# Kernel optimization log

Hardware: AMD Instinct MI355X
Metric: run time of the kernel (lower is better)

Reference implementation:

```python
import jax, jax.numpy as jnp
import numpy as np

NUM_HEADS = 10
LN_EPS = 1e-5

def setup_inputs() -> dict:
    key = jax.random.key(0)
    ks = jax.random.split(key, 8)
    B, H, N, D, Dt = 256, 200, 64, 640, 256
    s = 0.02
    return {
        'clicked_news': jax.random.normal(ks[0], (B, H, D), jnp.float32),
        'clicked_topics': jax.random.normal(ks[1], (B, H, Dt), jnp.float32),
        'cand_topics': jax.random.normal(ks[2], (B, N, Dt), jnp.float32),
        'Wq': jax.random.normal(ks[3], (D, Dt), jnp.float32) * s,
        'bq': jnp.zeros((D,), jnp.float32),
        'Wk': jax.random.normal(ks[4], (D, Dt), jnp.float32) * s,
        'bk': jnp.zeros((D,), jnp.float32),
        'Wv': jax.random.normal(ks[5], (D, D), jnp.float32) * s,
        'bv': jnp.zeros((D,), jnp.float32),
        'Wg': jax.random.normal(ks[6], (D, D), jnp.float32) * s,
        'bg': jnp.zeros((D,), jnp.float32),
        'ln_gamma': jnp.ones((D,), jnp.float32),
        'ln_beta': jnp.zeros((D,), jnp.float32),
    }

def reference(clicked_news, clicked_topics, cand_topics, Wq, bq, Wk, bk, Wv, bv, Wg, bg, ln_gamma, ln_beta):
    B, H, D = clicked_news.shape
    N = cand_topics.shape[1]
    nh = NUM_HEADS
    hd = D // nh
    scale = jnp.sqrt(jnp.asarray(D, clicked_news.dtype))

    Qf = cand_topics @ Wq.T + bq            # [B, N, D]
    Kf = clicked_topics @ Wk.T + bk         # [B, H, D]
    # V projection feeds `weighted`, which is dead code w.r.t. outputs; omitted.

    Q = Qf.reshape(B, N, nh, hd)
    K = Kf.reshape(B, H, nh, hd)
    scores = jnp.einsum('bnhd,bmhd->bhnm', Q, K) / scale   # [B, nh, N, H]
    attn = jax.nn.softmax(scores, axis=-1)                 # dropout is identity in eval

    # query weighting: softmax over candidates of ||Q||
    query_weights = jax.nn.softmax(jnp.linalg.norm(Qf, axis=-1), axis=1)   # [B, N]
    agg = (attn.sum(axis=1) * query_weights[:, :, None]).sum(axis=1)       # [B, H]
    attn_weights_agg = jax.nn.softmax(agg, axis=-1)                        # [B, H]

    weighted_clicked = attn_weights_agg[:, :, None] * clicked_news         # [B, H, D]
    gate = jax.nn.sigmoid(weighted_clicked @ Wg.T + bg)
    out = gate * weighted_clicked + (1.0 - gate) * clicked_news

    mu = out.mean(axis=-1, keepdims=True)
    var = out.var(axis=-1, keepdims=True)
    out = (out - mu) / jnp.sqrt(var + LN_EPS) * ln_gamma + ln_beta
    return out, attn_weights_agg
```

## Files before the change

kernel.cpp:

```cpp
#include <hip/hip_runtime.h>
#include <math.h>

#define B_  256
#define H_  200
#define N_  64
#define D_  640
#define DT_ 256
#define NH_ 10
#define HD_ 64
#define MT_ 13
#define MH_ 25600

typedef __attribute__((ext_vector_type(8))) short bf16x8;
typedef __attribute__((ext_vector_type(4))) float f32x4;

__device__ __forceinline__ float wave_reduce_sum(float v) {
    #pragma unroll
    for (int m = 32; m > 0; m >>= 1) v += __shfl_xor(v, m);
    return v;
}
__device__ __forceinline__ float wave_reduce_max(float v) {
    #pragma unroll
    for (int m = 32; m > 0; m >>= 1) v = fmaxf(v, __shfl_xor(v, m));
    return v;
}
__device__ __forceinline__ float red16_sum(float v) {
    #pragma unroll
    for (int m = 1; m < 16; m <<= 1) v += __shfl_xor(v, m);
    return v;
}
__device__ __forceinline__ float red16_max(float v) {
    #pragma unroll
    for (int m = 1; m < 16; m <<= 1) v = fmaxf(v, __shfl_xor(v, m));
    return v;
}
__device__ __forceinline__ short f2bf(float x) {
    unsigned u = __float_as_uint(x);
    unsigned r = (u + 0x7fffu + ((u >> 16) & 1u)) >> 16;
    return (short)r;
}
__device__ __forceinline__ float bf2f(short s) {
    return __uint_as_float(((unsigned)(unsigned short)s) << 16);
}

__device__ __forceinline__ void gload_lds16(const void* g, void* lds) {
    __builtin_amdgcn_global_load_lds(
        (const __attribute__((address_space(1))) void*)g,
        (__attribute__((address_space(3))) void*)lds, 16, 0, 0);
}

__global__ __launch_bounds__(256) void convert_w(
    const float* __restrict__ src, short* __restrict__ dst, int n)
{
    for (int i = blockIdx.x * 256 + threadIdx.x; i < n; i += gridDim.x * 256)
        dst[i] = f2bf(src[i]);
}

__global__ __launch_bounds__(256, 3) void gemm_bt(
    const float* __restrict__ A, int lda,
    const short* __restrict__ Wb, int ldb,
    const float* __restrict__ bias,
    short* __restrict__ Y, int nkc)
{
    __shared__ float A_f[128 * 64];
    __shared__ short B_lds[128 * 64];
    const int t = threadIdx.x;
    const int lane = t & 63, w = t >> 6;
    const int wm = w >> 1, wn = w & 1;
    const int r16 = lane & 15, g = lane >> 4;
    const int lb = (blockIdx.x & 7) * ((int)gridDim.x >> 3) + (blockIdx.x >> 3);
    const int row0 = (lb / 5) * 128;
    const int col0 = (lb % 5) * 128;

    f32x4 acc[4][4];
    #pragma unroll
    for (int ct = 0; ct < 4; ++ct)
        #pragma unroll
        for (int rt = 0; rt < 4; ++rt) acc[ct][rt] = (f32x4){0.f,0.f,0.f,0.f};

    for (int k = 0; k < nkc; ++k) {
        const int k0 = k * 64;
        #pragma unroll
        for (int j = 0; j < 8; ++j) {
            const int u = t + j * 256;
            const int row = u >> 4, jj = u & 15;
            gload_lds16(A + (long)(row0 + row) * lda + k0 + ((jj ^ (row & 7)) << 2),
                        (char*)A_f + u * 16);
        }
        #pragma unroll
        for (int j = 0; j < 4; ++j) {
            const int u = t + j * 256;
            const int col = u >> 3, jj = u & 7;
            gload_lds16(Wb + (long)(col0 + col) * ldb + k0 + ((jj ^ (col & 7)) << 3),
                        (char*)B_lds + u * 16);
        }
        __syncthreads();

        #pragma unroll
        for (int kk = 0; kk < 2; ++kk) {
            bf16x8 a[4];
            #pragma unroll
            for (int rt = 0; rt < 4; ++rt) {
                const int row = wm * 64 + rt * 16 + r16;
                const int s = kk * 8 + g * 2;
                float4 f0 = *(const float4*)(A_f + row * 64 + ((s ^ (row & 7)) << 2));
                float4 f1 = *(const float4*)(A_f + row * 64 + (((s + 1) ^ (row & 7)) << 2));
                bf16x8 av;
                av[0] = f2bf(f0.x); av[1] = f2bf(f0.y); av[2] = f2bf(f0.z); av[3] = f2bf(f0.w);
                av[4] = f2bf(f1.x); av[5] = f2bf(f1.y); av[6] = f2bf(f1.z); av[7] = f2bf(f1.w);
                a[rt] = av;
            }
            bf16x8 b[4];
            #pragma unroll
            for (int ct = 0; ct < 4; ++ct) {
                const int col = wn * 64 + ct * 16 + r16;
                const int sb = kk * 4 + g;
                b[ct] = *(const bf16x8*)(B_lds + col * 64 + ((sb ^ (col & 7)) << 3));
            }
            #pragma unroll
            for (int ct = 0; ct < 4; ++ct)
                #pragma unroll
                for (int rt = 0; rt < 4; ++rt)
                    acc[ct][rt] = __builtin_amdgcn_mfma_f32_16x16x32_bf16(
                                      a[rt], b[ct], acc[ct][rt], 0, 0, 0);
        }
        __syncthreads();
    }

    #pragma unroll
    for (int ct = 0; ct < 4; ++ct) {
        const int col = col0 + wn * 64 + ct * 16 + r16;
        const float bv = bias ? bias[col] : 0.f;
        #pragma unroll
        for (int rt = 0; rt < 4; ++rt)
            #pragma unroll
            for (int i = 0; i < 4; ++i)
                Y[(long)(row0 + wm * 64 + rt * 16 + g * 4 + i) * D_ + col] =
                    f2bf(acc[ct][rt][i] + bv);
    }
}

__global__ __launch_bounds__(512, 2) void attn2(
    const short* __restrict__ Qb, const short* __restrict__ Kb,
    float* __restrict__ aw, float* __restrict__ out_tail)
{
    __shared__ float qn_l[N_];
    __shared__ float qw_l[N_];
    __shared__ float aggp[8][MT_ * 16];
    __shared__ float red2[2];
    const int t = threadIdx.x;
    const int lane = t & 63, w = t >> 6;
    const int wm = w & 3, hh = w >> 2;
    const int r16 = lane & 15, g = lane >> 4;
    const int b = blockIdx.x;

    if (hh == 0) {
        const short* qrow = Qb + ((long)(b * N_ + wm * 16 + r16)) * D_ + g * 160;
        float ss = 0.f;
        #pragma unroll
        for (int j = 0; j < 20; ++j) {
            bf16x8 v = *(const bf16x8*)(qrow + j * 8);
            #pragma unroll
            for (int e = 0; e < 8; ++e) { float f = bf2f(v[e]); ss += f * f; }
        }
        ss += __shfl_xor(ss, 16);
        ss += __shfl_xor(ss, 32);
        if (g == 0) qn_l[wm * 16 + r16] = ss;
    }
    __syncthreads();
    if (w == 0) {
        float v = sqrtf(qn_l[lane]);
        float mx = wave_reduce_max(v);
        float e = __expf(v - mx);
        float s = wave_reduce_sum(e);
        qw_l[lane] = e / s;
    }
    __syncthreads();

    float qwr[4];
    #pragma unroll
    for (int i = 0; i < 4; ++i) qwr[i] = qw_l[wm * 16 + g * 4 + i];

    const float inv_scale = 0.0395284707521047f;
    float aggl[MT_];
    #pragma unroll
    for (int mt = 0; mt < MT_; ++mt) aggl[mt] = 0.f;

    for (int hi = 0; hi < 5; ++hi) {
        const int h = hh * 5 + hi;
        const short* qbase = Qb + ((long)(b * N_ + wm * 16 + r16)) * D_ + h * HD_ + g * 8;
        bf16x8 a0 = *(const bf16x8*)(qbase);
        bf16x8 a1 = *(const bf16x8*)(qbase + 32);
        bf16x8 kb0[MT_], kb1[MT_];
        #pragma unroll
        for (int mt = 0; mt < MT_; ++mt) {
            const short* kbase = Kb + ((long)(b * H_ + mt * 16 + r16)) * D_ + h * HD_ + g * 8;
            kb0[mt] = *(const bf16x8*)(kbase);
            kb1[mt] = *(const bf16x8*)(kbase + 32);
        }
        f32x4 acc[MT_];
        #pragma unroll
        for (int mt = 0; mt < MT_; ++mt) {
            f32x4 z = {0.f,0.f,0.f,0.f};
            z = __builtin_amdgcn_mfma_f32_16x16x32_bf16(a0, kb0[mt], z, 0, 0, 0);
            z = __builtin_amdgcn_mfma_f32_16x16x32_bf16(a1, kb1[mt], z, 0, 0, 0);
            acc[mt] = z;
        }
        const bool tailok = (r16 < 8);
        float mx[4] = {-INFINITY, -INFINITY, -INFINITY, -INFINITY};
        #pragma unroll
        for (int mt = 0; mt < MT_; ++mt) {
            const bool valid = (mt < 12) || tailok;
            #pragma unroll
            for (int i = 0; i < 4; ++i)
                if (valid) mx[i] = fmaxf(mx[i], acc[mt][i]);
        }
        #pragma unroll
        for (int i = 0; i < 4; ++i) mx[i] = red16_max(mx[i]);
        float sum[4] = {0.f, 0.f, 0.f, 0.f};
        #pragma unroll
        for (int mt = 0; mt < MT_; ++mt) {
            const bool valid = (mt < 12) || tailok;
            #pragma unroll
            for (int i = 0; i < 4; ++i) {
                float e = valid ? __expf((acc[mt][i] - mx[i]) * inv_scale) : 0.f;
                acc[mt][i] = e;
                sum[i] += e;
            }
        }
        float fct[4];
        #pragma unroll
        for (int i = 0; i < 4; ++i) fct[i] = qwr[i] / red16_sum(sum[i]);
        #pragma unroll
        for (int mt = 0; mt < MT_; ++mt)
            aggl[mt] += acc[mt][0] * fct[0] + acc[mt][1] * fct[1]
                      + acc[mt][2] * fct[2] + acc[mt][3] * fct[3];
    }
    #pragma unroll
    for (int mt = 0; mt < MT_; ++mt) {
        aggl[mt] += __shfl_xor(aggl[mt], 16);
        aggl[mt] += __shfl_xor(aggl[mt], 32);
    }
    if (g == 0) {
        #pragma unroll
        for (int mt = 0; mt < MT_; ++mt) aggp[w][mt * 16 + r16] = aggl[mt];
    }
    __syncthreads();
    if (t < MT_ * 16) {
        float v = 0.f;
        #pragma unroll
        for (int j = 0; j < 8; ++j) v += aggp[j][t];
        aggp[0][t] = v;
    }
    __syncthreads();
    if (w == 0) {
        float v0 = aggp[0][lane], v1 = aggp[0][lane + 64], v2 = aggp[0][lane + 128];
        const bool has3 = lane < (H_ - 192);
        float v3 = has3 ? aggp[0][lane + 192] : -INFINITY;
        float mx = wave_reduce_max(fmaxf(fmaxf(v0, v1), fmaxf(v2, v3)));
        float s = __expf(v0 - mx) + __expf(v1 - mx) + __expf(v2 - mx)
                + (has3 ? __expf(v3 - mx) : 0.f);
        s = wave_reduce_sum(s);
        if (lane == 0) { red2[0] = mx; red2[1] = s; }
    }
    __syncthreads();
    if (t < H_) {
        float v = __expf(aggp[0][t] - red2[0]) / red2[1];
        aw[b * H_ + t] = v;
        out_tail[b * H_ + t] = v;
    }
}

__global__ __launch_bounds__(256) void blendln(
    const float* __restrict__ cl, const short* __restrict__ Z,
    const float* __restrict__ aw, const float* __restrict__ bg,
    const float* __restrict__ gamma, const float* __restrict__ beta,
    float* __restrict__ out)
{
    const int t = threadIdx.x;
    const int lane = t & 63, w = t >> 6;
    const int row = blockIdx.x * 4 + w;
    const float awr = aw[row];
    const long base = (long)row * D_;

    float o[10];
    float s = 0.f, sq = 0.f;
    #pragma unroll
    for (int i = 0; i < 10; ++i) {
        const int col = lane + 64 * i;
        const float y = bf2f(Z[base + col]);
        const float c = cl[base + col];
        const float z = awr * y + bg[col];
        const float gt = 1.f / (1.f + __expf(-z));
        const float ov = c * (1.f + gt * (awr - 1.f));
        o[i] = ov; s += ov; sq += ov * ov;
    }
    s  = wave_reduce_sum(s);
    sq = wave_reduce_sum(sq);
    const float mu  = s * (1.f / D_);
    const float var = sq * (1.f / D_) - mu * mu;
    const float ri  = 1.0f / sqrtf(var + 1e-5f);
    #pragma unroll
    for (int i = 0; i < 10; ++i) {
        const int col = lane + 64 * i;
        out[base + col] = (o[i] - mu) * ri * gamma[col] + beta[col];
    }
}

extern "C" void kernel_launch(void* const* d_in, const int* in_sizes, int n_in,
                              void* d_out, int out_size, void* d_ws, size_t ws_size,
                              hipStream_t stream) {
    const float* clicked_news   = (const float*)d_in[0];
    const float* clicked_topics = (const float*)d_in[1];
    const float* cand_topics    = (const float*)d_in[2];
    const float* Wq = (const float*)d_in[3];
    const float* bq = (const float*)d_in[4];
    const float* Wk = (const float*)d_in[5];
    const float* bk = (const float*)d_in[6];
    const float* Wg = (const float*)d_in[9];
    const float* bg = (const float*)d_in[10];
    const float* ln_gamma = (const float*)d_in[11];
    const float* ln_beta  = (const float*)d_in[12];

    float* out = (float*)d_out;
    float* ws  = (float*)d_ws;

    float* aw   = ws;
    short* Wq_b = (short*)(aw + (long)B_ * H_);
    short* Wk_b = Wq_b + (long)D_ * DT_;
    short* Wg_b = Wk_b + (long)D_ * DT_;
    short* Qb   = Wg_b + (long)D_ * D_;
    short* Z    = Qb;
    short* Kb = (short*)d_out;
    float* out_tail = out + (long)B_ * H_ * D_;

    convert_w<<<128, 256, 0, stream>>>(Wq, Wq_b, D_ * DT_);
    convert_w<<<128, 256, 0, stream>>>(Wk, Wk_b, D_ * DT_);
    convert_w<<<256, 256, 0, stream>>>(Wg, Wg_b, D_ * D_);

    gemm_bt<<<640, 256, 0, stream>>>(cand_topics, DT_, Wq_b, DT_, bq, Qb, 4);
    gemm_bt<<<2000, 256, 0, stream>>>(clicked_topics, DT_, Wk_b, DT_, bk, Kb, 4);
    attn2<<<B_, 512, 0, stream>>>(Qb, Kb, aw, out_tail);

    for (int h = 0; h < 2; ++h) {
        const long off = (long)h * MH_;
        gemm_bt<<<1000, 256, 0, stream>>>(clicked_news + off * D_, D_,
                                          Wg_b, D_, nullptr, Z, 10);
        blendln<<<MH_ / 4, 256, 0, stream>>>(
            clicked_news + off * D_, Z, aw + off, bg, ln_gamma, ln_beta,
            out + off * D_);
    }
}
```

Measured before the change: 289.1 us.

## Double-buffer gemm_bt LDS tiles with half-size K chunks to overlap loads

The GEMM main loop now uses two LDS buffers with 32-wide K slices and prefetches the next slice while computing on the current one, with one barrier per iteration instead of two. The K chunk is halved so the total LDS footprint stays the same and occupancy is preserved, and call sites double the chunk count to match. The swizzle on the B tile changes for the narrower rows. The aim is to hide global-to-LDS load latency behind MFMA work, at the cost of twice as many loop iterations with fewer MFMAs each.

```diff
diff --git a/kernel.cpp b/kernel.cpp
--- a/kernel.cpp
+++ b/kernel.cpp
@@ -62,8 +62,8 @@
     const float* __restrict__ bias,
     short* __restrict__ Y, int nkc)
 {
-    __shared__ float A_f[128 * 64];
-    __shared__ short B_lds[128 * 64];
+    __shared__ float A_f[2][128 * 32];
+    __shared__ short B_l[2][128 * 32];
     const int t = threadIdx.x;
     const int lane = t & 63, w = t >> 6;
     const int wm = w >> 1, wn = w & 1;
@@ -78,52 +78,58 @@
         #pragma unroll
         for (int rt = 0; rt < 4; ++rt) acc[ct][rt] = (f32x4){0.f,0.f,0.f,0.f};
 
-    for (int k = 0; k < nkc; ++k) {
-        const int k0 = k * 64;
-        #pragma unroll
-        for (int j = 0; j < 8; ++j) {
-            const int u = t + j * 256;
-            const int row = u >> 4, jj = u & 15;
-            gload_lds16(A + (long)(row0 + row) * lda + k0 + ((jj ^ (row & 7)) << 2),
-                        (char*)A_f + u * 16);
-        }
+    auto STAGE = [&](int bi, int k) {
+        const int k0 = k * 32;
         #pragma unroll
         for (int j = 0; j < 4; ++j) {
             const int u = t + j * 256;
-            const int col = u >> 3, jj = u & 7;
-            gload_lds16(Wb + (long)(col0 + col) * ldb + k0 + ((jj ^ (col & 7)) << 3),
-                        (char*)B_lds + u * 16);
-        }
-        __syncthreads();
-
-        #pragma unroll
-        for (int kk = 0; kk < 2; ++kk) {
-            bf16x8 a[4];
-            #pragma unroll
-            for (int rt = 0; rt < 4; ++rt) {
-                const int row = wm * 64 + rt * 16 + r16;
-                const int s = kk * 8 + g * 2;
-                float4 f0 = *(const float4*)(A_f + row * 64 + ((s ^ (row & 7)) << 2));
-                float4 f1 = *(const float4*)(A_f + row * 64 + (((s + 1) ^ (row & 7)) << 2));
-                bf16x8 av;
-                av[0] = f2bf(f0.x); av[1] = f2bf(f0.y); av[2] = f2bf(f0.z); av[3] = f2bf(f0.w);
-                av[4] = f2bf(f1.x); av[5] = f2bf(f1.y); av[6] = f2bf(f1.z); av[7] = f2bf(f1.w);
-                a[rt] = av;
-            }
-            bf16x8 b[4];
-            #pragma unroll
-            for (int ct = 0; ct < 4; ++ct) {
-                const int col = wn * 64 + ct * 16 + r16;
-                const int sb = kk * 4 + g;
-                b[ct] = *(const bf16x8*)(B_lds + col * 64 + ((sb ^ (col & 7)) << 3));
-            }
-            #pragma unroll
-            for (int ct = 0; ct < 4; ++ct)
-                #pragma unroll
-                for (int rt = 0; rt < 4; ++rt)
-                    acc[ct][rt] = __builtin_amdgcn_mfma_f32_16x16x32_bf16(
-                                      a[rt], b[ct], acc[ct][rt], 0, 0, 0);
-        }
+            const int row = u >> 3, jj = u & 7;
+            gload_lds16(A + (long)(row0 + row) * lda + k0 + ((jj ^ (row & 7)) << 2),
+                        (char*)A_f[bi] + u * 16);
+        }
+        #pragma unroll
+        for (int j = 0; j < 2; ++j) {
+            const int u = t + j * 256;
+            const int col = u >> 2, jj = u & 3;
+            gload_lds16(Wb + (long)(col0 + col) * ldb + k0 + ((jj ^ ((col >> 1) & 3)) << 3),
+                        (char*)B_l[bi] + u * 16);
+        }
+    };
+
+    STAGE(0, 0);
+    __syncthreads();
+
+    for (int k = 0; k < nkc; ++k) {
+        if (k + 1 < nkc) STAGE((k + 1) & 1, k + 1);
+
+        const float* ab = A_f[k & 1];
+        const short* bb = B_l[k & 1];
+        bf16x8 a[4];
+        #pragma unroll
+        for (int rt = 0; rt < 4; ++rt) {
+            const int row = wm * 64 + rt * 16 + r16;
+            const int s0 = (g * 2) ^ (row & 7);
+            const int s1 = (g * 2 + 1) ^ (row & 7);
+            float4 f0 = *(const float4*)(ab + row * 32 + s0 * 4);
+            float4 f1 = *(const float4*)(ab + row * 32 + s1 * 4);
+            bf16x8 av;
+            av[0] = f2bf(f0.x); av[1] = f2bf(f0.y); av[2] = f2bf(f0.z); av[3] = f2bf(f0.w);
+            av[4] = f2bf(f1.x); av[5] = f2bf(f1.y); av[6] = f2bf(f1.z); av[7] = f2bf(f1.w);
+            a[rt] = av;
+        }
+        bf16x8 b[4];
+        #pragma unroll
+        for (int ct = 0; ct < 4; ++ct) {
+            const int col = wn * 64 + ct * 16 + r16;
+            const int sb = g ^ ((col >> 1) & 3);
+            b[ct] = *(const bf16x8*)(bb + col * 32 + sb * 8);
+        }
+        #pragma unroll
+        for (int ct = 0; ct < 4; ++ct)
+            #pragma unroll
+            for (int rt = 0; rt < 4; ++rt)
+                acc[ct][rt] = __builtin_amdgcn_mfma_f32_16x16x32_bf16(
+                                  a[rt], b[ct], acc[ct][rt], 0, 0, 0);
         __syncthreads();
     }
 
@@ -338,14 +344,14 @@
     convert_w<<<128, 256, 0, stream>>>(Wk, Wk_b, D_ * DT_);
     convert_w<<<256, 256, 0, stream>>>(Wg, Wg_b, D_ * D_);
 
-    gemm_bt<<<640, 256, 0, stream>>>(cand_topics, DT_, Wq_b, DT_, bq, Qb, 4);
-    gemm_bt<<<2000, 256, 0, stream>>>(clicked_topics, DT_, Wk_b, DT_, bk, Kb, 4);
+    gemm_bt<<<640, 256, 0, stream>>>(cand_topics, DT_, Wq_b, DT_, bq, Qb, 8);
+    gemm_bt<<<2000, 256, 0, stream>>>(clicked_topics, DT_, Wk_b, DT_, bk, Kb, 8);
     attn2<<<B_, 512, 0, stream>>>(Qb, Kb, aw, out_tail);
 
     for (int h = 0; h < 2; ++h) {
         const long off = (long)h * MH_;
         gemm_bt<<<1000, 256, 0, stream>>>(clicked_news + off * D_, D_,
-                                          Wg_b, D_, nullptr, Z, 10);
+                                          Wg_b, D_, nullptr, Z, 20);
         blendln<<<MH_ / 4, 256, 0, stream>>>(
             clicked_news + off * D_, Z, aw + off, bg, ln_gamma, ln_beta,
             out + off * D_);
```

After: 303.6 us. 1.05x slower.
